# Optimization experiments

Measured on AMD Instinct MI355X. Metric: run time of the kernel, lower is better.

The kernel has to match this reference:

```python
import jax, jax.numpy as jnp
import numpy as np

# ViT-B/16 CLIP visual tower dims
B, R, P = 32, 224, 16          # batch, resolution, patch
D, H, F, L = 768, 12, 3072, 12 # width, heads, mlp dim, layers
S = 1 + (R // P) ** 2          # 197 tokens (cls + patches)
O = 512                        # output proj dim
HD = D // H
MEAN = jnp.array([0.48145466, 0.4578275, 0.40821073], jnp.float32).reshape(1, 3, 1, 1)
STD = jnp.array([0.26862954, 0.26130258, 0.27577711], jnp.float32).reshape(1, 3, 1, 1)


def _ln(x, s, b):
    m = x.mean(-1, keepdims=True)
    v = ((x - m) ** 2).mean(-1, keepdims=True)
    return (x - m) * jax.lax.rsqrt(v + 1e-5) * s + b


def setup_inputs() -> dict:
    key = jax.random.key(0)
    ks = jax.random.split(key, 16)
    r = lambda i, shape: jax.random.normal(ks[i], shape, jnp.float32) * 0.02
    return dict(
        images=jax.random.uniform(ks[0], (B, 3, R, R), jnp.float32),
        conv_w=r(1, (D, 3, P, P)),
        cls_emb=r(2, (D,)),
        pos_emb=r(3, (S, D)),
        ln_pre_s=jnp.ones((D,), jnp.float32), ln_pre_b=jnp.zeros((D,), jnp.float32),
        ln1_s=jnp.ones((L, D), jnp.float32), ln1_b=jnp.zeros((L, D), jnp.float32),
        qkv_w=r(4, (L, 3 * D, D)), qkv_b=r(5, (L, 3 * D)),
        out_w=r(6, (L, D, D)), out_b=r(7, (L, D)),
        ln2_s=jnp.ones((L, D), jnp.float32), ln2_b=jnp.zeros((L, D), jnp.float32),
        fc_w=r(8, (L, F, D)), fc_b=r(9, (L, F)),
        proj_w=r(10, (L, D, F)), proj_b=r(11, (L, D)),
        ln_post_s=jnp.ones((D,), jnp.float32), ln_post_b=jnp.zeros((D,), jnp.float32),
        vis_proj=r(12, (D, O)),
    )


def reference(images, conv_w, cls_emb, pos_emb, ln_pre_s, ln_pre_b,
              ln1_s, ln1_b, qkv_w, qkv_b, out_w, out_b, ln2_s, ln2_b,
              fc_w, fc_b, proj_w, proj_b, ln_post_s, ln_post_b, vis_proj):
    x = (images - MEAN) / STD
    # conv1 patch embedding (no bias in CLIP): [B,D,14,14]
    x = jax.lax.conv_general_dilated(x, conv_w, (P, P), 'VALID',
                                     dimension_numbers=('NCHW', 'OIHW', 'NCHW'))
    x = x.reshape(B, D, -1).transpose(0, 2, 1)  # [B, 196, D]
    x = jnp.concatenate([jnp.broadcast_to(cls_emb, (B, 1, D)), x], axis=1) + pos_emb
    x = _ln(x, ln_pre_s, ln_pre_b)
    scale = HD ** -0.5

    def block(x, p):
        l1s, l1b, qw, qb, ow, ob, l2s, l2b, fw, fb, pw, pb = p
        h = _ln(x, l1s, l1b)
        qkv = h @ qw.T + qb                      # fused in_proj, [B,S,3D]
        q, k, v = jnp.split(qkv, 3, axis=-1)
        split = lambda t: t.reshape(B, S, H, HD).transpose(0, 2, 1, 3)
        q, k, v = split(q) * scale, split(k), split(v)
        attn = jax.nn.softmax(jnp.einsum('bhqd,bhkd->bhqk', q, k), axis=-1)
        o = jnp.einsum('bhqk,bhkd->bhqd', attn, v).transpose(0, 2, 1, 3).reshape(B, S, D)
        x = x + o @ ow.T + ob                    # out_proj + residual
        h = _ln(x, l2s, l2b) @ fw.T + fb
        h = h * jax.nn.sigmoid(1.702 * h)        # QuickGELU
        x = x + h @ pw.T + pb
        return x, None

    x, _ = jax.lax.scan(block, x, (ln1_s, ln1_b, qkv_w, qkv_b, out_w, out_b,
                                   ln2_s, ln2_b, fc_w, fc_b, proj_w, proj_b))
    x = _ln(x[:, 0], ln_post_s, ln_post_b)  # ln_post on cls token
    return x @ vis_proj                      # [B, 512]
```

## Files before the change

### kernel.cpp

```cpp
#include <hip/hip_runtime.h>
#include <cstddef>

#define Bv   32
#define Sv   197
#define Dv   768
#define Hh   12
#define HDv  64
#define Fv   3072
#define Lv   12
#define Ov   512
#define TOK  (Bv * Sv)
#define MPAD 6400
#define NPATCH 196
#define CONV_M (Bv * NPATCH)

#define WQ_SZ (2304 * 768)
#define WO_SZ (768 * 768)
#define WF_SZ (3072 * 768)
#define WP_SZ (768 * 3072)
#define WTOT  (WQ_SZ + WO_SZ + WF_SZ + WP_SZ)

typedef __attribute__((ext_vector_type(8))) __bf16 bf16x8;
typedef __attribute__((ext_vector_type(4))) float f32x4;

__device__ __forceinline__ unsigned short f2bf(float f) {
    unsigned int u = __float_as_uint(f);
    unsigned int r = (u + 0x7fffu + ((u >> 16) & 1u)) >> 16;
    return (unsigned short)r;
}

__device__ __forceinline__ void async_ld16(const void* g, void* l) {
    __builtin_amdgcn_global_load_lds(
        (__attribute__((address_space(1))) void*)(g),
        (__attribute__((address_space(3))) void*)(l),
        16, 0, 0);
}

__device__ __forceinline__ void reduce2_256(float& s1, float& s2) {
    #pragma unroll
    for (int off = 32; off > 0; off >>= 1) {
        s1 += __shfl_down(s1, off, 64);
        s2 += __shfl_down(s2, off, 64);
    }
    __shared__ float r1[4], r2[4];
    int lane = threadIdx.x & 63, w = threadIdx.x >> 6;
    if (lane == 0) { r1[w] = s1; r2[w] = s2; }
    __syncthreads();
    s1 = r1[0] + r1[1] + r1[2] + r1[3];
    s2 = r2[0] + r2[1] + r2[2] + r2[3];
    __syncthreads();
}

__global__ void convert_kernel(const float* __restrict__ src,
                               unsigned short* __restrict__ dst, int n4) {
    int gid = blockIdx.x * 256 + threadIdx.x;
    if (gid >= n4) return;
    int idx = gid * 4;
    float4 v = *(const float4*)(src + idx);
    ushort4 r = make_ushort4(f2bf(v.x), f2bf(v.y), f2bf(v.z), f2bf(v.w));
    *(ushort4*)(dst + idx) = r;
}

__global__ void convertw_kernel(const float* __restrict__ wq,
                                const float* __restrict__ wo,
                                const float* __restrict__ wf,
                                const float* __restrict__ wp,
                                unsigned short* __restrict__ dst) {
    int idx = (blockIdx.x * 256 + threadIdx.x) * 4;
    const float* s; int off;
    if (idx < WQ_SZ)                     { s = wq; off = idx; }
    else if (idx < WQ_SZ + WO_SZ)        { s = wo; off = idx - WQ_SZ; }
    else if (idx < WQ_SZ + WO_SZ + WF_SZ){ s = wf; off = idx - WQ_SZ - WO_SZ; }
    else                                 { s = wp; off = idx - WQ_SZ - WO_SZ - WF_SZ; }
    float4 v = *(const float4*)(s + off);
    ushort4 r = make_ushort4(f2bf(v.x), f2bf(v.y), f2bf(v.z), f2bf(v.w));
    *(ushort4*)(dst + idx) = r;
}

__global__ void im2col_kernel(const float* __restrict__ img,
                              unsigned short* __restrict__ out) {
    int idx = blockIdx.x * 256 + threadIdx.x;
    int col = idx % 768;
    int row = idx / 768;
    int b = row / NPATCH, p = row % NPATCH;
    int ph = p / 14, pw = p % 14;
    int c  = col >> 8;
    int r  = col & 255;
    int kh = r >> 4, kw = r & 15;
    int y = ph * 16 + kh, x = pw * 16 + kw;
    const float mean[3] = {0.48145466f, 0.4578275f, 0.40821073f};
    const float stdv[3] = {0.26862954f, 0.26130258f, 0.27577711f};
    float v = img[((size_t)(b * 3 + c) * 224 + y) * 224 + x];
    out[idx] = f2bf((v - mean[c]) / stdv[c]);
}

template<int ODT, int ACT>
__global__ __launch_bounds__(256) void gemm_mfma(
        const unsigned short* __restrict__ A, const unsigned short* __restrict__ W,
        const float* __restrict__ bias, const float* __restrict__ res,
        void* __restrict__ Cv, int M, int N, int K)
{
    __shared__ unsigned short As[3][128 * 32];
    __shared__ unsigned short Ws[3][128 * 32];
    const int tid = threadIdx.x;
    const int w = tid >> 6, l = tid & 63;

    const int gx = gridDim.x;
    const int wg  = blockIdx.y * gx + blockIdx.x;
    const int nwg = gx * gridDim.y;
    const int q = nwg >> 3, r8 = nwg & 7;
    const int xcd = wg & 7, lo = wg >> 3;
    const int swz = (xcd < r8 ? xcd * (q + 1) : r8 * (q + 1) + (xcd - r8) * q) + lo;
    const int m0 = (swz / gx) << 7;
    const int n0 = (swz % gx) << 7;

    const int srow = w * 32 + (l >> 2);
    const int scol = (l & 3) * 8;
    const unsigned short* ag0 = A + (size_t)(m0 + srow) * K + scol;
    const unsigned short* ag1 = ag0 + (size_t)16 * K;
    const unsigned short* wg0 = W + (size_t)(n0 + srow) * K + scol;
    const unsigned short* wg1 = wg0 + (size_t)16 * K;

    const int wm = w >> 1, wn = w & 1;
    const int fr = l & 15, fq = l >> 4;
    int aoff[4], woff[4];
    #pragma unroll
    for (int i = 0; i < 4; i++) {
        aoff[i] = (wm * 64 + i * 16 + fr) * 32 + fq * 8;
        woff[i] = (wn * 64 + i * 16 + fr) * 32 + fq * 8;
    }

    f32x4 acc[4][4] = {};
    const int nk = K >> 5;

    #define STAGE(t, buf) do {                                      \
        const int _ko = (t) << 5;                                   \
        async_ld16(ag0 + _ko, &As[buf][w * 1024]);                  \
        async_ld16(ag1 + _ko, &As[buf][w * 1024 + 512]);            \
        async_ld16(wg0 + _ko, &Ws[buf][w * 1024]);                  \
        async_ld16(wg1 + _ko, &Ws[buf][w * 1024 + 512]);            \
    } while (0)

    auto compute = [&](const unsigned short* ab, const unsigned short* wb) {
        bf16x8 af[4], wf[4];
        #pragma unroll
        for (int i = 0; i < 4; i++) {
            af[i] = *(const bf16x8*)(ab + aoff[i]);
            wf[i] = *(const bf16x8*)(wb + woff[i]);
        }
        #pragma unroll
        for (int i = 0; i < 4; i++) {
            #pragma unroll
            for (int j = 0; j < 4; j++) {
                acc[i][j] = __builtin_amdgcn_mfma_f32_16x16x32_bf16(
                    af[i], wf[j], acc[i][j], 0, 0, 0);
            }
        }
    };

    STAGE(0, 0);
    STAGE(1, 1);

    for (int kk = 0; kk < nk - 1; kk++) {
        asm volatile("s_waitcnt vmcnt(4)" ::: "memory");
        __builtin_amdgcn_s_barrier();
        if (kk + 2 < nk) STAGE(kk + 2, (kk + 2) % 3);
        compute(As[kk % 3], Ws[kk % 3]);
    }
    asm volatile("s_waitcnt vmcnt(0)" ::: "memory");
    __builtin_amdgcn_s_barrier();
    compute(As[(nk - 1) % 3], Ws[(nk - 1) % 3]);

    #undef STAGE

    float bn[4];
    #pragma unroll
    for (int j = 0; j < 4; j++)
        bn[j] = bias ? bias[n0 + wn * 64 + j * 16 + fr] : 0.f;

    #pragma unroll
    for (int i = 0; i < 4; i++) {
        #pragma unroll
        for (int r = 0; r < 4; r++) {
            int m = m0 + wm * 64 + i * 16 + fq * 4 + r;
            if (m < M) {
                size_t rowb = (size_t)m * N;
                #pragma unroll
                for (int j = 0; j < 4; j++) {
                    int n = n0 + wn * 64 + j * 16 + fr;
                    float v = acc[i][j][r] + bn[j];
                    if (res) v += res[rowb + n];
                    if (ACT) v = v / (1.f + __expf(-1.702f * v));
                    if (ODT == 0) ((float*)Cv)[rowb + n] = v;
                    else ((unsigned short*)Cv)[rowb + n] = f2bf(v);
                }
            }
        }
    }
}

__global__ void ln_kernel(const float* __restrict__ in, unsigned short* __restrict__ out,
                          const float* __restrict__ s, const float* __restrict__ b) {
    int t = blockIdx.x;
    const float* row = in + (size_t)t * Dv;
    int tid = threadIdx.x;
    float v[3], s1 = 0.f, s2 = 0.f;
    #pragma unroll
    for (int i = 0; i < 3; i++) {
        v[i] = row[tid + 256 * i];
        s1 += v[i]; s2 += v[i] * v[i];
    }
    reduce2_256(s1, s2);
    float mean = s1 * (1.0f / Dv);
    float var  = s2 * (1.0f / Dv) - mean * mean;
    float rstd = rsqrtf(var + 1e-5f);
    unsigned short* orow = out + (size_t)t * Dv;
    #pragma unroll
    for (int i = 0; i < 3; i++) {
        int d = tid + 256 * i;
        orow[d] = f2bf((v[i] - mean) * rstd * s[d] + b[d]);
    }
}

__global__ void embed_ln_kernel(const float* __restrict__ conv_out,
                                const float* __restrict__ cls,
                                const float* __restrict__ pos,
                                const float* __restrict__ s,
                                const float* __restrict__ b,
                                float* __restrict__ x) {
    int t = blockIdx.x;
    int bb = t / Sv, si = t % Sv;
    int tid = threadIdx.x;
    float v[3], s1 = 0.f, s2 = 0.f;
    #pragma unroll
    for (int i = 0; i < 3; i++) {
        int d = tid + 256 * i;
        float e = (si == 0) ? cls[d]
                            : conv_out[((size_t)bb * NPATCH + (si - 1)) * Dv + d];
        v[i] = e + pos[(size_t)si * Dv + d];
        s1 += v[i]; s2 += v[i] * v[i];
    }
    reduce2_256(s1, s2);
    float mean = s1 * (1.0f / Dv);
    float var  = s2 * (1.0f / Dv) - mean * mean;
    float rstd = rsqrtf(var + 1e-5f);
    float* orow = x + (size_t)t * Dv;
    #pragma unroll
    for (int i = 0; i < 3; i++) {
        int d = tid + 256 * i;
        orow[d] = (v[i] - mean) * rstd * s[d] + b[d];
    }
}

__global__ __launch_bounds__(256) void attn4_kernel(
        const unsigned short* __restrict__ qkv, unsigned short* __restrict__ o) {
    const int qg = blockIdx.x, h = blockIdx.y, b = blockIdx.z;
    __shared__ __align__(16) unsigned short vt[64][232];
    __shared__ __align__(16) unsigned short pb[32][236];
    __shared__ float red[4][32];
    __shared__ float smax_f[32];
    __shared__ float sinv_f[32];

    const int tid = threadIdx.x;
    const int w = tid >> 6, l = tid & 63;
    const int fr = l & 15, fq = l >> 4;
    const size_t base = (size_t)b * Sv;
    const unsigned int* q32 = (const unsigned int*)qkv;

    for (int i = tid; i < 224 * 32; i += 256) {
        int j = i >> 5, u = i & 31;
        unsigned int val = (j < Sv) ? q32[(base + j) * 1152 + 768 + h * 32 + u] : 0u;
        vt[2 * u][j]     = (unsigned short)(val & 0xffffu);
        vt[2 * u + 1][j] = (unsigned short)(val >> 16);
    }

    union U { uint4 u; bf16x8 v; };

    f32x4 sc[2][4] = {};
    #pragma unroll
    for (int ks = 0; ks < 2; ks++) {
        U aq[2];
        #pragma unroll
        for (int mt = 0; mt < 2; mt++) {
            int row = qg * 32 + mt * 16 + fr;
            int rc = row < Sv ? row : Sv - 1;
            aq[mt].u = *(const uint4*)(qkv + (base + rc) * 2304 + h * 64 + ks * 32 + fq * 8);
        }
        #pragma unroll
        for (int s = 0; s < 4; s++) {
            int nt = w + 4 * s;
            if (nt >= 14) continue;
            int col = nt * 16 + fr;
            int cc = col < Sv ? col : Sv - 1;
            U bq;
            bq.u = *(const uint4*)(qkv + (base + cc) * 2304 + 768 + h * 64 + ks * 32 + fq * 8);
            #pragma unroll
            for (int mt = 0; mt < 2; mt++)
                sc[mt][s] = __builtin_amdgcn_mfma_f32_16x16x32_bf16(
                    aq[mt].v, bq.v, sc[mt][s], 0, 0, 0);
        }
    }

    float rmax[2][4];
    #pragma unroll
    for (int mt = 0; mt < 2; mt++)
        #pragma unroll
        for (int r = 0; r < 4; r++) rmax[mt][r] = -1e30f;
    #pragma unroll
    for (int mt = 0; mt < 2; mt++) {
        #pragma unroll
        for (int s = 0; s < 4; s++) {
            int nt = w + 4 * s;
            int col = nt * 16 + fr;
            bool valid = (nt < 14) && (col < Sv);
            #pragma unroll
            for (int r = 0; r < 4; r++) {
                float v = valid ? sc[mt][s][r] * 0.125f : -1e30f;
                sc[mt][s][r] = v;
                rmax[mt][r] = fmaxf(rmax[mt][r], v);
            }
        }
    }
    #pragma unroll
    for (int mt = 0; mt < 2; mt++) {
        #pragma unroll
        for (int r = 0; r < 4; r++) {
            float m = rmax[mt][r];
            m = fmaxf(m, __shfl_xor(m, 1, 64));
            m = fmaxf(m, __shfl_xor(m, 2, 64));
            m = fmaxf(m, __shfl_xor(m, 4, 64));
            m = fmaxf(m, __shfl_xor(m, 8, 64));
            rmax[mt][r] = m;
        }
    }
    if (fr == 0) {
        #pragma unroll
        for (int mt = 0; mt < 2; mt++)
            #pragma unroll
            for (int r = 0; r < 4; r++)
                red[w][mt * 16 + fq * 4 + r] = rmax[mt][r];
    }
    __syncthreads();
    if (tid < 32)
        smax_f[tid] = fmaxf(fmaxf(red[0][tid], red[1][tid]),
                            fmaxf(red[2][tid], red[3][tid]));
    __syncthreads();

    float rsum[2][4] = {};
    #pragma unroll
    for (int mt = 0; mt < 2; mt++) {
        float fm[4];
        #pragma unroll
        for (int r = 0; r < 4; r++) fm[r] = smax_f[mt * 16 + fq * 4 + r];
        #pragma unroll
        for (int s = 0; s < 4; s++) {
            int nt = w + 4 * s;
            if (nt >= 14) continue;
            int col = nt * 16 + fr;
            #pragma unroll
            for (int r = 0; r < 4; r++) {
                float p = (col < Sv) ? __expf(sc[mt][s][r] - fm[r]) : 0.f;
                rsum[mt][r] += p;
                pb[mt * 16 + fq * 4 + r][col] = f2bf(p);
            }
        }
    }
    #pragma unroll
    for (int mt = 0; mt < 2; mt++) {
        #pragma unroll
        for (int r = 0; r < 4; r++) {
            float s = rsum[mt][r];
            s += __shfl_xor(s, 1, 64);
            s += __shfl_xor(s, 2, 64);
            s += __shfl_xor(s, 4, 64);
            s += __shfl_xor(s, 8, 64);
            rsum[mt][r] = s;
        }
    }
    if (fr == 0) {
        #pragma unroll
        for (int mt = 0; mt < 2; mt++)
            #pragma unroll
            for (int r = 0; r < 4; r++)
                red[w][mt * 16 + fq * 4 + r] = rsum[mt][r];
    }
    __syncthreads();
    if (tid < 32)
        sinv_f[tid] = 1.f / (red[0][tid] + red[1][tid] + red[2][tid] + red[3][tid]);
    __syncthreads();

    f32x4 oc[2] = {};
    #pragma unroll
    for (int ks = 0; ks < 7; ks++) {
        U bv;
        bv.u = *(const uint4*)&vt[w * 16 + fr][ks * 32 + fq * 8];
        #pragma unroll
        for (int mt = 0; mt < 2; mt++) {
            const unsigned short* ap = &pb[mt * 16 + fr][ks * 32 + fq * 8];
            uint2 lo = *(const uint2*)ap;
            uint2 hi = *(const uint2*)(ap + 4);
            U a; a.u = make_uint4(lo.x, lo.y, hi.x, hi.y);
            oc[mt] = __builtin_amdgcn_mfma_f32_16x16x32_bf16(a.v, bv.v, oc[mt], 0, 0, 0);
        }
    }

    #pragma unroll
    for (int mt = 0; mt < 2; mt++) {
        #pragma unroll
        for (int r = 0; r < 4; r++) {
            int lrow = mt * 16 + fq * 4 + r;
            int row = qg * 32 + lrow;
            if (row < Sv)
                o[(base + row) * Dv + h * 64 + w * 16 + fr] =
                    f2bf(oc[mt][r] * sinv_f[lrow]);
        }
    }
}

__global__ void head_kernel(const float* __restrict__ x,
                            const float* __restrict__ s, const float* __restrict__ b,
                            const float* __restrict__ vp, float* __restrict__ out) {
    int bb = blockIdx.x, tid = threadIdx.x;
    __shared__ float xn[Dv];
    const float* row = x + (size_t)(bb * Sv) * Dv;
    float v[3], s1 = 0.f, s2 = 0.f;
    #pragma unroll
    for (int i = 0; i < 3; i++) {
        v[i] = row[tid + 256 * i];
        s1 += v[i]; s2 += v[i] * v[i];
    }
    reduce2_256(s1, s2);
    float mean = s1 * (1.0f / Dv);
    float var  = s2 * (1.0f / Dv) - mean * mean;
    float rstd = rsqrtf(var + 1e-5f);
    #pragma unroll
    for (int i = 0; i < 3; i++) {
        int d = tid + 256 * i;
        xn[d] = (v[i] - mean) * rstd * s[d] + b[d];
    }
    __syncthreads();
    float acc0 = 0.f, acc1 = 0.f;
    for (int d = 0; d < Dv; d++) {
        float xv = xn[d];
        acc0 += xv * vp[(size_t)d * Ov + tid];
        acc1 += xv * vp[(size_t)d * Ov + tid + 256];
    }
    out[(size_t)bb * Ov + tid]       = acc0;
    out[(size_t)bb * Ov + tid + 256] = acc1;
}

extern "C" void kernel_launch(void* const* d_in, const int* in_sizes, int n_in,
                              void* d_out, int out_size, void* d_ws, size_t ws_size,
                              hipStream_t stream) {
    const float* images   = (const float*)d_in[0];
    const float* conv_w   = (const float*)d_in[1];
    const float* cls_emb  = (const float*)d_in[2];
    const float* pos_emb  = (const float*)d_in[3];
    const float* lnpre_s  = (const float*)d_in[4];
    const float* lnpre_b  = (const float*)d_in[5];
    const float* ln1_s    = (const float*)d_in[6];
    const float* ln1_b    = (const float*)d_in[7];
    const float* qkv_w    = (const float*)d_in[8];
    const float* qkv_b    = (const float*)d_in[9];
    const float* out_w    = (const float*)d_in[10];
    const float* out_b    = (const float*)d_in[11];
    const float* ln2_s    = (const float*)d_in[12];
    const float* ln2_b    = (const float*)d_in[13];
    const float* fc_w     = (const float*)d_in[14];
    const float* fc_b     = (const float*)d_in[15];
    const float* proj_w   = (const float*)d_in[16];
    const float* proj_b   = (const float*)d_in[17];
    const float* lnpost_s = (const float*)d_in[18];
    const float* lnpost_b = (const float*)d_in[19];
    const float* vis_proj = (const float*)d_in[20];
    float* out = (float*)d_out;

    char* p = (char*)d_ws;
    float* x              = (float*)p;          p += (size_t)TOK * Dv * 4;
    unsigned short* abuf  = (unsigned short*)p; p += (size_t)MPAD * Dv * 2;
    unsigned short* qkvb  = (unsigned short*)p; p += (size_t)MPAD * 2304 * 2;
    unsigned short* hbuf  = (unsigned short*)p; p += (size_t)MPAD * Fv * 2;
    unsigned short* wbuf  = (unsigned short*)p; p += (size_t)WTOT * 2;
    unsigned short* cwb   = (unsigned short*)p; p += (size_t)WO_SZ * 2;
    unsigned short* im2c  = qkvb;
    float* convo          = (float*)hbuf;

    convert_kernel<<<WO_SZ / 4 / 256, 256, 0, stream>>>(conv_w, cwb, WO_SZ / 4);
    im2col_kernel<<<(CONV_M * Dv) / 256, 256, 0, stream>>>(images, im2c);
    gemm_mfma<0, 0><<<dim3(Dv / 128, CONV_M / 128), 256, 0, stream>>>(
        im2c, cwb, nullptr, nullptr, convo, CONV_M, Dv, Dv);
    embed_ln_kernel<<<TOK, 256, 0, stream>>>(convo, cls_emb, pos_emb,
                                             lnpre_s, lnpre_b, x);

    unsigned short* wq = wbuf;
    unsigned short* wo = wbuf + WQ_SZ;
    unsigned short* wf = wbuf + WQ_SZ + WO_SZ;
    unsigned short* wp = wbuf + WQ_SZ + WO_SZ + WF_SZ;
    const int GM = MPAD / 128;

    for (int l = 0; l < Lv; l++) {
        convertw_kernel<<<WTOT / 4 / 256, 256, 0, stream>>>(
            qkv_w + (size_t)l * WQ_SZ, out_w + (size_t)l * WO_SZ,
            fc_w + (size_t)l * WF_SZ, proj_w + (size_t)l * WP_SZ, wbuf);
        ln_kernel<<<TOK, 256, 0, stream>>>(x, abuf, ln1_s + l * Dv, ln1_b + l * Dv);
        gemm_mfma<1, 0><<<dim3(2304 / 128, GM), 256, 0, stream>>>(
            abuf, wq, qkv_b + (size_t)l * 2304, nullptr, qkvb, TOK, 2304, Dv);
        attn4_kernel<<<dim3(7, Hh, Bv), 256, 0, stream>>>(qkvb, abuf);
        gemm_mfma<0, 0><<<dim3(Dv / 128, GM), 256, 0, stream>>>(
            abuf, wo, out_b + (size_t)l * Dv, x, x, TOK, Dv, Dv);
        ln_kernel<<<TOK, 256, 0, stream>>>(x, abuf, ln2_s + l * Dv, ln2_b + l * Dv);
        gemm_mfma<1, 1><<<dim3(Fv / 128, GM), 256, 0, stream>>>(
            abuf, wf, fc_b + (size_t)l * Fv, nullptr, hbuf, TOK, Fv, Dv);
        gemm_mfma<0, 0><<<dim3(Dv / 128, GM), 256, 0, stream>>>(
            hbuf, wp, proj_b + (size_t)l * Dv, x, x, TOK, Dv, Fv);
    }

    head_kernel<<<Bv, 256, 0, stream>>>(x, lnpost_s, lnpost_b, vis_proj, out);
}
```

Baseline: 4.088 ms.

## Retile GEMM to 256x128 blocks with 512 threads, K-step 64, swizzled LDS

The bf16 MFMA GEMM moves from 128x128 tiles with 256 threads and a 3-stage 32-deep K pipeline to 256x128 tiles with 512 threads and a 2-stage 64-deep K pipeline. Global-to-LDS loads use an XOR-swizzled chunk layout, and the fragment reads apply the matching swizzle to avoid LDS bank conflicts. The larger tile raises arithmetic intensity and halves barriers per K. In exchange it halves the workgroup count, leaving the 768-wide GEMMs with only 150 blocks on a 256-CU device, and it drains all loads (vmcnt(0)) before each barrier, which reduces load/compute overlap.

```diff
diff --git a/kernel.cpp b/kernel.cpp
--- a/kernel.cpp
+++ b/kernel.cpp
@@ -95,13 +95,13 @@
 }
 
 template<int ODT, int ACT>
-__global__ __launch_bounds__(256) void gemm_mfma(
+__global__ __launch_bounds__(512) void gemm_mfma(
         const unsigned short* __restrict__ A, const unsigned short* __restrict__ W,
         const float* __restrict__ bias, const float* __restrict__ res,
         void* __restrict__ Cv, int M, int N, int K)
 {
-    __shared__ unsigned short As[3][128 * 32];
-    __shared__ unsigned short Ws[3][128 * 32];
+    __shared__ unsigned short As[2][256 * 64];
+    __shared__ unsigned short Ws[2][128 * 64];
     const int tid = threadIdx.x;
     const int w = tid >> 6, l = tid & 63;
 
@@ -111,66 +111,77 @@
     const int q = nwg >> 3, r8 = nwg & 7;
     const int xcd = wg & 7, lo = wg >> 3;
     const int swz = (xcd < r8 ? xcd * (q + 1) : r8 * (q + 1) + (xcd - r8) * q) + lo;
-    const int m0 = (swz / gx) << 7;
+    const int m0 = (swz / gx) << 8;
     const int n0 = (swz % gx) << 7;
 
-    const int srow = w * 32 + (l >> 2);
-    const int scol = (l & 3) * 8;
-    const unsigned short* ag0 = A + (size_t)(m0 + srow) * K + scol;
-    const unsigned short* ag1 = ag0 + (size_t)16 * K;
-    const unsigned short* wg0 = W + (size_t)(n0 + srow) * K + scol;
-    const unsigned short* wg1 = wg0 + (size_t)16 * K;
+    const int lrow = l >> 3;
+    const int lchk = (l & 7) ^ lrow;
+    const unsigned short* agp = A + (size_t)(m0 + w * 8 + lrow) * K + lchk * 8;
+    const unsigned short* wgp = W + (size_t)(n0 + w * 8 + lrow) * K + lchk * 8;
+    const int lbase = (w * 8) * 64;
 
     const int wm = w >> 1, wn = w & 1;
     const int fr = l & 15, fq = l >> 4;
-    int aoff[4], woff[4];
-    #pragma unroll
-    for (int i = 0; i < 4; i++) {
-        aoff[i] = (wm * 64 + i * 16 + fr) * 32 + fq * 8;
-        woff[i] = (wn * 64 + i * 16 + fr) * 32 + fq * 8;
+    int aoff[2][4], woff[2][4];
+    #pragma unroll
+    for (int ks = 0; ks < 2; ks++) {
+        const int pc = ((ks * 4 + fq) ^ (fr & 7)) * 8;
+        #pragma unroll
+        for (int i = 0; i < 4; i++) {
+            aoff[ks][i] = (wm * 64 + i * 16 + fr) * 64 + pc;
+            woff[ks][i] = (wn * 64 + i * 16 + fr) * 64 + pc;
+        }
     }
 
     f32x4 acc[4][4] = {};
-    const int nk = K >> 5;
-
-    #define STAGE(t, buf) do {                                      \
-        const int _ko = (t) << 5;                                   \
-        async_ld16(ag0 + _ko, &As[buf][w * 1024]);                  \
-        async_ld16(ag1 + _ko, &As[buf][w * 1024 + 512]);            \
-        async_ld16(wg0 + _ko, &Ws[buf][w * 1024]);                  \
-        async_ld16(wg1 + _ko, &Ws[buf][w * 1024 + 512]);            \
+    const int nt = K >> 6;
+
+    #define STAGE(t, bf) do {                                              \
+        const int _ko = (t) << 6;                                          \
+        _Pragma("unroll")                                                  \
+        for (int _i = 0; _i < 4; _i++)                                     \
+            async_ld16(agp + (size_t)_i * 64 * K + _ko,                    \
+                       &As[bf][lbase + _i * 64 * 64]);                     \
+        _Pragma("unroll")                                                  \
+        for (int _i = 0; _i < 2; _i++)                                     \
+            async_ld16(wgp + (size_t)_i * 64 * K + _ko,                    \
+                       &Ws[bf][lbase + _i * 64 * 64]);                     \
     } while (0)
 
     auto compute = [&](const unsigned short* ab, const unsigned short* wb) {
-        bf16x8 af[4], wf[4];
-        #pragma unroll
-        for (int i = 0; i < 4; i++) {
-            af[i] = *(const bf16x8*)(ab + aoff[i]);
-            wf[i] = *(const bf16x8*)(wb + woff[i]);
-        }
-        #pragma unroll
-        for (int i = 0; i < 4; i++) {
-            #pragma unroll
-            for (int j = 0; j < 4; j++) {
-                acc[i][j] = __builtin_amdgcn_mfma_f32_16x16x32_bf16(
-                    af[i], wf[j], acc[i][j], 0, 0, 0);
+        #pragma unroll
+        for (int ks = 0; ks < 2; ks++) {
+            bf16x8 af[4], wf[4];
+            #pragma unroll
+            for (int i = 0; i < 4; i++) {
+                af[i] = *(const bf16x8*)(ab + aoff[ks][i]);
+                wf[i] = *(const bf16x8*)(wb + woff[ks][i]);
             }
+            #pragma unroll
+            for (int i = 0; i < 4; i++) {
+                #pragma unroll
+                for (int j = 0; j < 4; j++) {
+                    acc[i][j] = __builtin_amdgcn_mfma_f32_16x16x32_bf16(
+                        af[i], wf[j], acc[i][j], 0, 0, 0);
+                }
+            }
         }
     };
 
     STAGE(0, 0);
-    STAGE(1, 1);
-
-    for (int kk = 0; kk < nk - 1; kk++) {
-        asm volatile("s_waitcnt vmcnt(4)" ::: "memory");
-        __builtin_amdgcn_s_barrier();
-        if (kk + 2 < nk) STAGE(kk + 2, (kk + 2) % 3);
-        compute(As[kk % 3], Ws[kk % 3]);
-    }
     asm volatile("s_waitcnt vmcnt(0)" ::: "memory");
     __builtin_amdgcn_s_barrier();
-    compute(As[(nk - 1) % 3], Ws[(nk - 1) % 3]);
-
+
+    int bf = 0;
+    for (int t = 0; t < nt; t++) {
+        if (t + 1 < nt) STAGE(t + 1, bf ^ 1);
+        compute(As[bf], Ws[bf]);
+        if (t + 1 < nt) {
+            asm volatile("s_waitcnt vmcnt(0)" ::: "memory");
+            __builtin_amdgcn_s_barrier();
+            bf ^= 1;
+        }
+    }
     #undef STAGE
 
     float bn[4];
@@ -485,9 +496,11 @@
     unsigned short* im2c  = qkvb;
     float* convo          = (float*)hbuf;
 
+    const int GY = MPAD / 256;
+
     convert_kernel<<<WO_SZ / 4 / 256, 256, 0, stream>>>(conv_w, cwb, WO_SZ / 4);
     im2col_kernel<<<(CONV_M * Dv) / 256, 256, 0, stream>>>(images, im2c);
-    gemm_mfma<0, 0><<<dim3(Dv / 128, CONV_M / 128), 256, 0, stream>>>(
+    gemm_mfma<0, 0><<<dim3(Dv / 128, GY), 512, 0, stream>>>(
         im2c, cwb, nullptr, nullptr, convo, CONV_M, Dv, Dv);
     embed_ln_kernel<<<TOK, 256, 0, stream>>>(convo, cls_emb, pos_emb,
                                              lnpre_s, lnpre_b, x);
@@ -496,22 +509,21 @@
     unsigned short* wo = wbuf + WQ_SZ;
     unsigned short* wf = wbuf + WQ_SZ + WO_SZ;
     unsigned short* wp = wbuf + WQ_SZ + WO_SZ + WF_SZ;
-    const int GM = MPAD / 128;
 
     for (int l = 0; l < Lv; l++) {
         convertw_kernel<<<WTOT / 4 / 256, 256, 0, stream>>>(
             qkv_w + (size_t)l * WQ_SZ, out_w + (size_t)l * WO_SZ,
             fc_w + (size_t)l * WF_SZ, proj_w + (size_t)l * WP_SZ, wbuf);
         ln_kernel<<<TOK, 256, 0, stream>>>(x, abuf, ln1_s + l * Dv, ln1_b + l * Dv);
-        gemm_mfma<1, 0><<<dim3(2304 / 128, GM), 256, 0, stream>>>(
+        gemm_mfma<1, 0><<<dim3(2304 / 128, GY), 512, 0, stream>>>(
             abuf, wq, qkv_b + (size_t)l * 2304, nullptr, qkvb, TOK, 2304, Dv);
         attn4_kernel<<<dim3(7, Hh, Bv), 256, 0, stream>>>(qkvb, abuf);
-        gemm_mfma<0, 0><<<dim3(Dv / 128, GM), 256, 0, stream>>>(
+        gemm_mfma<0, 0><<<dim3(Dv / 128, GY), 512, 0, stream>>>(
             abuf, wo, out_b + (size_t)l * Dv, x, x, TOK, Dv, Dv);
         ln_kernel<<<TOK, 256, 0, stream>>>(x, abuf, ln2_s + l * Dv, ln2_b + l * Dv);
-        gemm_mfma<1, 1><<<dim3(Fv / 128, GM), 256, 0, stream>>>(
+        gemm_mfma<1, 1><<<dim3(Fv / 128, GY), 512, 0, stream>>>(
             abuf, wf, fc_b + (size_t)l * Fv, nullptr, hbuf, TOK, Fv, Dv);
-        gemm_mfma<0, 0><<<dim3(Dv / 128, GM), 256, 0, stream>>>(
+        gemm_mfma<0, 0><<<dim3(Dv / 128, GY), 512, 0, stream>>>(
             hbuf, wp, proj_b + (size_t)l * Dv, x, x, TOK, Dv, Fv);
     }
 
```

Result: slower. 4.255 ms (+4.1%).
